# Optimization experiments

Measured on AMD Instinct MI355X. Metric: run time of the kernel, lower is better.

The kernel has to match this reference:

```python
import jax, jax.numpy as jnp
import numpy as np

N = 100000
E = 1600000
IN_DIM = 32
LATENT = 64
K = 3          # num_hops
L = 5          # num_layers


def setup_inputs() -> dict:
    key = jax.random.key(0)
    ks = jax.random.split(key, 8)
    x = jax.random.normal(ks[0], (N, IN_DIM), dtype=jnp.float32)
    edge_index = jax.random.randint(ks[1], (2, E), 0, N, dtype=jnp.int64)
    edge_weight = jax.random.uniform(ks[2], (E,), dtype=jnp.float32)
    # TAGConv params: per layer, (K+1) hop-wise linear weights + one bias
    s0 = 1.0 / np.sqrt(IN_DIM)
    s1 = 1.0 / np.sqrt(LATENT)
    W0 = jax.random.uniform(ks[3], (K + 1, IN_DIM, LATENT), jnp.float32, -s0, s0)
    b0 = jnp.zeros((LATENT,), jnp.float32)
    Ws = jax.random.uniform(ks[4], (L - 1, K + 1, LATENT, LATENT), jnp.float32, -s1, s1)
    bs = jnp.zeros((L - 1, LATENT), jnp.float32)
    return {"x": x, "edge_index": edge_index, "edge_weight": edge_weight,
            "W0": W0, "b0": b0, "Ws": Ws, "bs": bs}


def _gcn_norm(edge_index, edge_weight, num_nodes):
    # TAGConv uses gcn_norm with add_self_loops=False (symmetric normalization)
    row, col = edge_index[0], edge_index[1]
    deg = jax.ops.segment_sum(edge_weight, col, num_segments=num_nodes)
    safe = jnp.where(deg > 0, deg, 1.0)
    dinv = jnp.where(deg > 0, 1.0 / jnp.sqrt(safe), 0.0)
    return dinv[row] * edge_weight * dinv[col]


def _tagconv(x, row, col, norm, W, b, num_nodes):
    # out = sum_{k=0}^{K} (A_hat^k x) @ W[k] + b
    out = x @ W[0]
    h = x
    for k in range(1, W.shape[0]):
        h = jax.ops.segment_sum(norm[:, None] * h[row], col, num_segments=num_nodes)
        out = out + h @ W[k]
    return out + b


def reference(x, edge_index, edge_weight, W0, b0, Ws, bs):
    row, col = edge_index[0], edge_index[1]
    norm = _gcn_norm(edge_index, edge_weight, N)
    h = jax.nn.relu(_tagconv(x, row, col, norm, W0, b0, N))
    for i in range(Ws.shape[0]):
        h = jax.nn.relu(_tagconv(h, row, col, norm, Ws[i], bs[i], N))
    return h
```

## Files before the change

### kernel.cpp

```cpp
#include <hip/hip_runtime.h>
#include <hip/hip_fp16.h>

#define NN 100000
#define NE 1600000
#define NBKT 196
#define BSH 9
#define BCAP 9216
#define NCOL (NBKT * 512)
#define EPB_A 4096

typedef __half half_t;
using f16x8 = __attribute__((ext_vector_type(8))) _Float16;
using f32x4 = __attribute__((ext_vector_type(4))) float;


__device__ inline float4 load4(const float* p) {
    return *reinterpret_cast<const float4*>(p);
}
__device__ inline float4 load4(const half_t* p) {
    uint2 u = *reinterpret_cast<const uint2*>(p);
    __half2 a = *reinterpret_cast<__half2*>(&u.x);
    __half2 b = *reinterpret_cast<__half2*>(&u.y);
    float2 fa = __half22float2(a), fb = __half22float2(b);
    return make_float4(fa.x, fa.y, fb.x, fb.y);
}
__device__ inline void store_half4(half_t* p, float4 v) {
    __half2 a = __floats2half2_rn(v.x, v.y);
    __half2 b = __floats2half2_rn(v.z, v.w);
    uint2 u;
    u.x = *reinterpret_cast<unsigned*>(&a);
    u.y = *reinterpret_cast<unsigned*>(&b);
    *reinterpret_cast<uint2*>(p) = u;
}


__global__ void f32_to_f16(const float* __restrict__ in, half_t* __restrict__ out, int nquad) {
    int i = blockIdx.x * blockDim.x + threadIdx.x;
    if (i < nquad) store_half4(out + i * 4, load4(in + i * 4));
}

__global__ __launch_bounds__(256) void passA_bucket(
    const int* __restrict__ row, const int* __restrict__ col, const float* __restrict__ w,
    unsigned* __restrict__ gcur, int2* __restrict__ gbkt, int E)
{
    __shared__ unsigned cnt[256];
    __shared__ unsigned lofs[256];
    __shared__ unsigned lcur[256];
    __shared__ unsigned gb[256];
    __shared__ int2 arena[EPB_A];
    __shared__ unsigned short abkt[EPB_A];
    int t = threadIdx.x;
    int base = blockIdx.x * EPB_A;
    int nloc = min(EPB_A, E - base);
    cnt[t] = 0; lcur[t] = 0;
    __syncthreads();
    for (int i = t; i < nloc; i += 256)
        atomicAdd(&cnt[col[base + i] >> BSH], 1u);
    __syncthreads();
    unsigned v = cnt[t];
    lofs[t] = v; __syncthreads();
    for (int d = 1; d < 256; d <<= 1) {
        unsigned u = (t >= d) ? lofs[t - d] : 0u;
        __syncthreads();
        lofs[t] += u;
        __syncthreads();
    }
    unsigned excl = lofs[t] - v;
    __syncthreads();
    lofs[t] = excl;
    __syncthreads();
    if (t < NBKT && cnt[t] > 0) gb[t] = atomicAdd(&gcur[t], cnt[t]);
    for (int i = t; i < nloc; i += 256) {
        int e = base + i;
        int c = col[e];
        int b = c >> BSH;
        unsigned p = lofs[b] + atomicAdd(&lcur[b], 1u);
        unsigned packed = ((unsigned)(c & 511) << 17) | (unsigned)row[e];
        arena[p] = make_int2((int)packed, __float_as_int(w[e]));
        abkt[p] = (unsigned short)b;
    }
    __syncthreads();
    for (int i = t; i < nloc; i += 256) {
        int b = abkt[i];
        unsigned j = i - lofs[b];
        gbkt[(size_t)b * BCAP + gb[b] + j] = arena[i];
    }
}

__global__ __launch_bounds__(256) void passB_hist(
    const int2* __restrict__ gbkt, const unsigned* __restrict__ gcur,
    unsigned* __restrict__ cnt, float* __restrict__ deg)
{
    __shared__ unsigned c512[512];
    __shared__ float d512[512];
    int t = threadIdx.x;
    int b = blockIdx.x;
    for (int i = t; i < 512; i += 256) { c512[i] = 0; d512[i] = 0.f; }
    __syncthreads();
    unsigned sz = min(gcur[b], (unsigned)BCAP);
    const int2* src = gbkt + (size_t)b * BCAP;
    for (unsigned i = t; i < sz; i += 256) {
        int2 v = src[i];
        unsigned colw = ((unsigned)v.x) >> 17;
        atomicAdd(&c512[colw], 1u);
        atomicAdd(&d512[colw], __int_as_float(v.y));
    }
    __syncthreads();
    for (int i = t; i < 512; i += 256) {
        cnt[b * 512 + i] = c512[i];
        deg[b * 512 + i] = d512[i];
    }
}

__global__ void dinv_kernel(const float* __restrict__ deg, float* __restrict__ dinv, int n) {
    int i = blockIdx.x * blockDim.x + threadIdx.x;
    if (i < n) {
        float d = deg[i];
        dinv[i] = d > 0.f ? rsqrtf(d) : 0.f;
    }
}

__global__ void scan_phase1(const unsigned* __restrict__ cnt, unsigned* __restrict__ bsum, int n) {
    __shared__ unsigned sh[256];
    int t = threadIdx.x;
    int base = blockIdx.x * 1024 + t * 4;
    unsigned s = 0;
#pragma unroll
    for (int j = 0; j < 4; j++) { int i = base + j; if (i < n) s += cnt[i]; }
    sh[t] = s; __syncthreads();
    for (int d = 128; d > 0; d >>= 1) {
        if (t < d) sh[t] += sh[t + d];
        __syncthreads();
    }
    if (t == 0) bsum[blockIdx.x] = sh[0];
}

__global__ void scan_phase2(const unsigned* __restrict__ bsum, unsigned* __restrict__ bbase, int nb) {
    __shared__ unsigned sh[128];
    int t = threadIdx.x;
    unsigned v = (t < nb) ? bsum[t] : 0u;
    sh[t] = v; __syncthreads();
    for (int d = 1; d < 128; d <<= 1) {
        unsigned u = (t >= d) ? sh[t - d] : 0u;
        __syncthreads();
        sh[t] += u;
        __syncthreads();
    }
    if (t < nb) bbase[t] = sh[t] - v;
}

__global__ void scan_phase3(const unsigned* __restrict__ cnt, const unsigned* __restrict__ bbase,
                            unsigned* __restrict__ offsets, int n) {
    __shared__ unsigned sh[256];
    int t = threadIdx.x;
    int base = blockIdx.x * 1024 + t * 4;
    unsigned c[4]; unsigned s = 0;
#pragma unroll
    for (int j = 0; j < 4; j++) { int i = base + j; c[j] = (i < n) ? cnt[i] : 0u; s += c[j]; }
    sh[t] = s; __syncthreads();
    for (int d = 1; d < 256; d <<= 1) {
        unsigned u = (t >= d) ? sh[t - d] : 0u;
        __syncthreads();
        sh[t] += u;
        __syncthreads();
    }
    unsigned o = bbase[blockIdx.x] + sh[t] - s;
#pragma unroll
    for (int j = 0; j < 4; j++) {
        int i = base + j;
        if (i < n) { offsets[i] = o; o += c[j]; }
    }
}

__global__ __launch_bounds__(256) void passC_place(
    const int2* __restrict__ gbkt, const unsigned* __restrict__ gcur,
    const unsigned* __restrict__ offsets, const float* __restrict__ dinv,
    int2* __restrict__ ent)
{
    __shared__ unsigned lcur[512];
    int t = threadIdx.x;
    int b = blockIdx.x;
    for (int i = t; i < 512; i += 256) lcur[i] = 0;
    __syncthreads();
    unsigned sz = min(gcur[b], (unsigned)BCAP);
    const int2* src = gbkt + (size_t)b * BCAP;
    for (unsigned i = t; i < sz; i += 256) {
        int2 v = src[i];
        unsigned colw = ((unsigned)v.x) >> 17;
        int r = v.x & 0x1FFFF;
        int c = (b << BSH) | (int)colw;
        unsigned pos = offsets[c] + atomicAdd(&lcur[colw], 1u);
        float wv = __int_as_float(v.y) * dinv[r];
        ent[pos] = make_int2(r, __float_as_int(wv));
    }
}


template <int DIM, typename SrcT>
__global__ __launch_bounds__(256) void spmm_kernel(
    const SrcT* __restrict__ src, half_t* __restrict__ pout,
    const int2* __restrict__ ent, const unsigned* __restrict__ offs,
    const unsigned* __restrict__ cnt, const float* __restrict__ dinv, int n)
{
    constexpr int TPN = DIM / 4;
    constexpr int NPB = 256 / TPN;
    int node = blockIdx.x * NPB + threadIdx.x / TPN;
    int f = (threadIdx.x % TPN) * 4;
    if (node >= n) return;
    unsigned off = offs[node];
    unsigned c = cnt[node];
    float dv = dinv[node];
    float4 a = {0.f, 0.f, 0.f, 0.f};
#pragma unroll 2
    for (unsigned e = off; e < off + c; ++e) {
        int2 en = ent[e];
        float w = __int_as_float(en.y);
        float4 v = load4(src + (size_t)en.x * DIM + f);
        a.x += w * v.x; a.y += w * v.y; a.z += w * v.z; a.w += w * v.w;
    }
    a.x *= dv; a.y *= dv; a.z *= dv; a.w *= dv;
    store_half4(pout + (size_t)node * DIM + f, a);
}


__global__ __launch_bounds__(256) void spmm64_kernel(
    const half_t* __restrict__ src, half_t* __restrict__ pout,
    const int2* __restrict__ ent, const unsigned* __restrict__ offs,
    const unsigned* __restrict__ cnt, const float* __restrict__ dinv, int n)
{
    int node = blockIdx.x * 32 + (threadIdx.x >> 3);
    int f = (threadIdx.x & 7) * 8;
    if (node >= n) return;
    unsigned off = offs[node], c = cnt[node];
    float dv = dinv[node];
    float acc[8] = {};
#pragma unroll 2
    for (unsigned e = off; e < off + c; ++e) {
        int2 en = ent[e];
        float w = __int_as_float(en.y);
        uint4 raw = *reinterpret_cast<const uint4*>(src + (size_t)en.x * 64 + f);
        __half2* h2 = reinterpret_cast<__half2*>(&raw);
#pragma unroll
        for (int j = 0; j < 4; ++j) {
            float2 v = __half22float2(h2[j]);
            acc[2 * j]     += w * v.x;
            acc[2 * j + 1] += w * v.y;
        }
    }
    uint4 o;
    __half2 h;
    h = __floats2half2_rn(acc[0] * dv, acc[1] * dv); o.x = *reinterpret_cast<unsigned*>(&h);
    h = __floats2half2_rn(acc[2] * dv, acc[3] * dv); o.y = *reinterpret_cast<unsigned*>(&h);
    h = __floats2half2_rn(acc[4] * dv, acc[5] * dv); o.z = *reinterpret_cast<unsigned*>(&h);
    h = __floats2half2_rn(acc[6] * dv, acc[7] * dv); o.w = *reinterpret_cast<unsigned*>(&h);
    *reinterpret_cast<uint4*>(pout + (size_t)node * 64 + f) = o;
}


template <int IN, int MODE>
__global__ __launch_bounds__(256) void fused4_mfma(
    const half_t* __restrict__ A0, const half_t* __restrict__ P1,
    const half_t* __restrict__ P2, const half_t* __restrict__ P3,
    const float* __restrict__ W, const float* __restrict__ bias,
    half_t* __restrict__ hdst, float* __restrict__ fdst, int n)
{
    constexpr int KK  = IN / 32;
    constexpr int WTS = IN + 8;
    __shared__ _Float16 Wt[64][WTS];
    int t = threadIdx.x;
    int w = t >> 6, l = t & 63;
    int nodeBase = blockIdx.x * 64;
    int rowTop = nodeBase + w * 16;

    f32x4 acc[4];
#pragma unroll
    for (int ct = 0; ct < 4; ++ct) acc[ct] = (f32x4){0.f, 0.f, 0.f, 0.f};

    int row = rowTop + (l & 15);
    if (row >= n) row = n - 1;
    const int khome = (l >> 4) * 8;

#pragma unroll
    for (int s = 0; s < 4; ++s) {
        const half_t* S = (s == 0) ? A0 : (s == 1) ? P1 : (s == 2) ? P2 : P3;
        const float* Wsrc = W + s * IN * 64;
        for (int idx = t; idx < IN * 64; idx += 256) {
            int k = idx >> 6, colj = idx & 63;
            Wt[colj][k] = (_Float16)Wsrc[idx];
        }
        __syncthreads();
#pragma unroll
        for (int kk = 0; kk < KK; ++kk) {
            uint4 araw = *reinterpret_cast<const uint4*>(S + (size_t)row * IN + kk * 32 + khome);
            f16x8 afrag = __builtin_bit_cast(f16x8, araw);
#pragma unroll
            for (int ct = 0; ct < 4; ++ct) {
                f16x8 bfrag = *reinterpret_cast<const f16x8*>(&Wt[ct * 16 + (l & 15)][kk * 32 + khome]);
                acc[ct] = __builtin_amdgcn_mfma_f32_16x16x32_f16(afrag, bfrag, acc[ct], 0, 0, 0);
            }
        }
        __syncthreads();
    }

    int colb = l & 15;
    int rbase = rowTop + (l >> 4) * 4;
#pragma unroll
    for (int ct = 0; ct < 4; ++ct) {
#pragma unroll
        for (int r = 0; r < 4; ++r) {
            int node = rbase + r;
            if (node >= n) continue;
            int colj = ct * 16 + colb;
            float v = fmaxf(acc[ct][r] + bias[colj], 0.f);
            size_t o = (size_t)node * 64 + colj;
            if (MODE == 1) hdst[o] = __float2half_rn(v);
            else           fdst[o] = v;
        }
    }
}


extern "C" void kernel_launch(void* const* d_in, const int* in_sizes, int n_in,
                              void* d_out, int out_size, void* d_ws, size_t ws_size,
                              hipStream_t stream) {
    const float* x  = (const float*)d_in[0];
    const int*   ei = (const int*)d_in[1];
    const float* ew = (const float*)d_in[2];
    const float* W0 = (const float*)d_in[3];
    const float* b0 = (const float*)d_in[4];
    const float* Ws = (const float*)d_in[5];
    const float* bs = (const float*)d_in[6];
    float* out = (float*)d_out;

    const int* row = ei;
    const int* col = ei + NE;

    char* wsp = (char*)d_ws;
    auto alloc = [&](size_t bytes) -> char* {
        char* p = wsp;
        wsp += (bytes + 255) & ~(size_t)255;
        return p;
    };
    float*    dinv    = (float*)alloc((size_t)NCOL * 4);
    float*    deg     = (float*)alloc((size_t)NCOL * 4);
    unsigned* cnt     = (unsigned*)alloc((size_t)NCOL * 4);
    unsigned* offsets = (unsigned*)alloc((size_t)NCOL * 4);
    unsigned* bsum    = (unsigned*)alloc(256 * 4);
    unsigned* bbase   = (unsigned*)alloc(256 * 4);
    unsigned* gcur    = (unsigned*)alloc(NBKT * 4);
    int2*     ent     = (int2*)alloc((size_t)NE * 8);
    half_t*   xh      = (half_t*)alloc((size_t)NN * 32 * 2);
    half_t*   B0      = (half_t*)alloc((size_t)NN * 64 * 2);
    half_t*   P1      = (half_t*)alloc((size_t)NN * 64 * 2);
    half_t*   P2      = (half_t*)alloc((size_t)NN * 64 * 2);
    half_t*   P3      = (half_t*)alloc((size_t)NN * 64 * 2);
    int2*     gbkt    = (int2*)P1;

    hipMemsetAsync(gcur, 0, NBKT * 4, stream);

    f32_to_f16<<<(NN * 32 / 4 + 255) / 256, 256, 0, stream>>>(x, xh, NN * 32 / 4);

    const int AB = (NE + EPB_A - 1) / EPB_A;
    passA_bucket<<<AB, 256, 0, stream>>>(row, col, ew, gcur, gbkt, NE);
    passB_hist<<<NBKT, 256, 0, stream>>>(gbkt, gcur, cnt, deg);
    dinv_kernel<<<(NN + 255) / 256, 256, 0, stream>>>(deg, dinv, NN);
    const int NB = NCOL / 1024;
    scan_phase1<<<NB, 256, 0, stream>>>(cnt, bsum, NCOL);
    scan_phase2<<<1, 128, 0, stream>>>(bsum, bbase, NB);
    scan_phase3<<<NB, 256, 0, stream>>>(cnt, bbase, offsets, NCOL);
    passC_place<<<NBKT, 256, 0, stream>>>(gbkt, gcur, offsets, dinv, ent);

    const int MMB  = (NN + 63) / 64;
    const int SB32 = (NN + 31) / 32;
    const int SB64 = (NN + 31) / 32;

    spmm_kernel<32, float><<<SB32, 256, 0, stream>>>(x, P1, ent, offsets, cnt, dinv, NN);
    spmm_kernel<32, half_t><<<SB32, 256, 0, stream>>>(P1, P2, ent, offsets, cnt, dinv, NN);
    spmm_kernel<32, half_t><<<SB32, 256, 0, stream>>>(P2, P3, ent, offsets, cnt, dinv, NN);
    fused4_mfma<32, 1><<<MMB, 256, 0, stream>>>(xh, P1, P2, P3, W0, b0, B0, nullptr, NN);

    for (int l = 0; l < 4; ++l) {
        const float* Wl = Ws + (size_t)l * 4 * 64 * 64;
        const float* bl = bs + (size_t)l * 64;
        spmm64_kernel<<<SB64, 256, 0, stream>>>(B0, P1, ent, offsets, cnt, dinv, NN);
        spmm64_kernel<<<SB64, 256, 0, stream>>>(P1, P2, ent, offsets, cnt, dinv, NN);
        spmm64_kernel<<<SB64, 256, 0, stream>>>(P2, P3, ent, offsets, cnt, dinv, NN);
        if (l < 3)
            fused4_mfma<64, 1><<<MMB, 256, 0, stream>>>(B0, P1, P2, P3, Wl, bl, B0, nullptr, NN);
        else
            fused4_mfma<64, 2><<<MMB, 256, 0, stream>>>(B0, P1, P2, P3, Wl, bl, nullptr, out, NN);
    }
}
```

Measured before the change: 664.1 us.

## Sort nodes by in-degree to balance SpMM warp workloads

Adds a degree histogram, a scan and a permutation-build pass that order nodes into buckets by in-degree (capped at 63). All SpMM kernels then process nodes through this permutation, so the nodes sharing a wavefront have similar edge counts and less lane divergence in the edge loop. The cost is three extra small kernels, an indirection load per node, and scattered output writes, which lose the locality of nodes being stored in index order.

```diff
diff --git a/kernel.cpp b/kernel.cpp
--- a/kernel.cpp
+++ b/kernel.cpp
@@ -196,17 +196,64 @@
 }
 
 
-template <int DIM, typename SrcT>
-__global__ __launch_bounds__(256) void spmm_kernel(
+__global__ __launch_bounds__(256) void deg_hist(const unsigned* __restrict__ cnt,
+                                                unsigned* __restrict__ dhist, int n) {
+    __shared__ unsigned h[64];
+    int t = threadIdx.x;
+    if (t < 64) h[t] = 0;
+    __syncthreads();
+    int i = blockIdx.x * 256 + t;
+    if (i < n) atomicAdd(&h[min(cnt[i], 63u)], 1u);
+    __syncthreads();
+    if (t < 64 && h[t]) atomicAdd(&dhist[t], h[t]);
+}
+
+__global__ void deg_scan(const unsigned* __restrict__ dhist, unsigned* __restrict__ dcur) {
+    __shared__ unsigned sh[64];
+    int t = threadIdx.x;
+    unsigned v = dhist[t];
+    sh[t] = v; __syncthreads();
+    for (int d = 1; d < 64; d <<= 1) {
+        unsigned u = (t >= d) ? sh[t - d] : 0u;
+        __syncthreads();
+        sh[t] += u;
+        __syncthreads();
+    }
+    dcur[t] = sh[t] - v;
+}
+
+__global__ __launch_bounds__(256) void perm_build(const unsigned* __restrict__ cnt,
+                                                  unsigned* __restrict__ dcur,
+                                                  int* __restrict__ perm, int n) {
+    __shared__ unsigned h[64], gb[64], lc[64];
+    int t = threadIdx.x;
+    if (t < 64) { h[t] = 0; lc[t] = 0; }
+    __syncthreads();
+    int i = blockIdx.x * 256 + t;
+    bool valid = i < n;
+    unsigned b = 0;
+    if (valid) { b = min(cnt[i], 63u); atomicAdd(&h[b], 1u); }
+    __syncthreads();
+    if (t < 64 && h[t]) gb[t] = atomicAdd(&dcur[t], h[t]);
+    __syncthreads();
+    if (valid) {
+        unsigned r = atomicAdd(&lc[b], 1u);
+        perm[gb[b] + r] = i;
+    }
+}
+
+
+template <typename SrcT>
+__global__ __launch_bounds__(256) void spmm32_kernel(
     const SrcT* __restrict__ src, half_t* __restrict__ pout,
     const int2* __restrict__ ent, const unsigned* __restrict__ offs,
-    const unsigned* __restrict__ cnt, const float* __restrict__ dinv, int n)
-{
-    constexpr int TPN = DIM / 4;
-    constexpr int NPB = 256 / TPN;
-    int node = blockIdx.x * NPB + threadIdx.x / TPN;
-    int f = (threadIdx.x % TPN) * 4;
-    if (node >= n) return;
+    const unsigned* __restrict__ cnt, const float* __restrict__ dinv,
+    const int* __restrict__ perm, int n)
+{
+    int s = blockIdx.x * 32 + (threadIdx.x >> 3);
+    int f = (threadIdx.x & 7) * 4;
+    if (s >= n) return;
+    int node = perm[s];
     unsigned off = offs[node];
     unsigned c = cnt[node];
     float dv = dinv[node];
@@ -215,22 +262,24 @@
     for (unsigned e = off; e < off + c; ++e) {
         int2 en = ent[e];
         float w = __int_as_float(en.y);
-        float4 v = load4(src + (size_t)en.x * DIM + f);
+        float4 v = load4(src + (size_t)en.x * 32 + f);
         a.x += w * v.x; a.y += w * v.y; a.z += w * v.z; a.w += w * v.w;
     }
     a.x *= dv; a.y *= dv; a.z *= dv; a.w *= dv;
-    store_half4(pout + (size_t)node * DIM + f, a);
+    store_half4(pout + (size_t)node * 32 + f, a);
 }
 
 
 __global__ __launch_bounds__(256) void spmm64_kernel(
     const half_t* __restrict__ src, half_t* __restrict__ pout,
     const int2* __restrict__ ent, const unsigned* __restrict__ offs,
-    const unsigned* __restrict__ cnt, const float* __restrict__ dinv, int n)
-{
-    int node = blockIdx.x * 32 + (threadIdx.x >> 3);
+    const unsigned* __restrict__ cnt, const float* __restrict__ dinv,
+    const int* __restrict__ perm, int n)
+{
+    int s = blockIdx.x * 32 + (threadIdx.x >> 3);
     int f = (threadIdx.x & 7) * 8;
-    if (node >= n) return;
+    if (s >= n) return;
+    int node = perm[s];
     unsigned off = offs[node], c = cnt[node];
     float dv = dinv[node];
     float acc[8] = {};
@@ -345,9 +394,12 @@
     float*    deg     = (float*)alloc((size_t)NCOL * 4);
     unsigned* cnt     = (unsigned*)alloc((size_t)NCOL * 4);
     unsigned* offsets = (unsigned*)alloc((size_t)NCOL * 4);
+    int*      perm    = (int*)alloc((size_t)NN * 4);
     unsigned* bsum    = (unsigned*)alloc(256 * 4);
     unsigned* bbase   = (unsigned*)alloc(256 * 4);
     unsigned* gcur    = (unsigned*)alloc(NBKT * 4);
+    unsigned* dhist   = (unsigned*)alloc(64 * 4);
+    unsigned* dcur    = (unsigned*)alloc(64 * 4);
     int2*     ent     = (int2*)alloc((size_t)NE * 8);
     half_t*   xh      = (half_t*)alloc((size_t)NN * 32 * 2);
     half_t*   B0      = (half_t*)alloc((size_t)NN * 64 * 2);
@@ -357,6 +409,7 @@
     int2*     gbkt    = (int2*)P1;
 
     hipMemsetAsync(gcur, 0, NBKT * 4, stream);
+    hipMemsetAsync(dhist, 0, 64 * 4, stream);
 
     f32_to_f16<<<(NN * 32 / 4 + 255) / 256, 256, 0, stream>>>(x, xh, NN * 32 / 4);
 
@@ -364,27 +417,30 @@
     passA_bucket<<<AB, 256, 0, stream>>>(row, col, ew, gcur, gbkt, NE);
     passB_hist<<<NBKT, 256, 0, stream>>>(gbkt, gcur, cnt, deg);
     dinv_kernel<<<(NN + 255) / 256, 256, 0, stream>>>(deg, dinv, NN);
+    const int PB = (NN + 255) / 256;
+    deg_hist<<<PB, 256, 0, stream>>>(cnt, dhist, NN);
+    deg_scan<<<1, 64, 0, stream>>>(dhist, dcur);
+    perm_build<<<PB, 256, 0, stream>>>(cnt, dcur, perm, NN);
     const int NB = NCOL / 1024;
     scan_phase1<<<NB, 256, 0, stream>>>(cnt, bsum, NCOL);
     scan_phase2<<<1, 128, 0, stream>>>(bsum, bbase, NB);
     scan_phase3<<<NB, 256, 0, stream>>>(cnt, bbase, offsets, NCOL);
     passC_place<<<NBKT, 256, 0, stream>>>(gbkt, gcur, offsets, dinv, ent);
 
-    const int MMB  = (NN + 63) / 64;
-    const int SB32 = (NN + 31) / 32;
-    const int SB64 = (NN + 31) / 32;
-
-    spmm_kernel<32, float><<<SB32, 256, 0, stream>>>(x, P1, ent, offsets, cnt, dinv, NN);
-    spmm_kernel<32, half_t><<<SB32, 256, 0, stream>>>(P1, P2, ent, offsets, cnt, dinv, NN);
-    spmm_kernel<32, half_t><<<SB32, 256, 0, stream>>>(P2, P3, ent, offsets, cnt, dinv, NN);
+    const int MMB = (NN + 63) / 64;
+    const int SB  = (NN + 31) / 32;
+
+    spmm32_kernel<float><<<SB, 256, 0, stream>>>(x, P1, ent, offsets, cnt, dinv, perm, NN);
+    spmm32_kernel<half_t><<<SB, 256, 0, stream>>>(P1, P2, ent, offsets, cnt, dinv, perm, NN);
+    spmm32_kernel<half_t><<<SB, 256, 0, stream>>>(P2, P3, ent, offsets, cnt, dinv, perm, NN);
     fused4_mfma<32, 1><<<MMB, 256, 0, stream>>>(xh, P1, P2, P3, W0, b0, B0, nullptr, NN);
 
     for (int l = 0; l < 4; ++l) {
         const float* Wl = Ws + (size_t)l * 4 * 64 * 64;
         const float* bl = bs + (size_t)l * 64;
-        spmm64_kernel<<<SB64, 256, 0, stream>>>(B0, P1, ent, offsets, cnt, dinv, NN);
-        spmm64_kernel<<<SB64, 256, 0, stream>>>(P1, P2, ent, offsets, cnt, dinv, NN);
-        spmm64_kernel<<<SB64, 256, 0, stream>>>(P2, P3, ent, offsets, cnt, dinv, NN);
+        spmm64_kernel<<<SB, 256, 0, stream>>>(B0, P1, ent, offsets, cnt, dinv, perm, NN);
+        spmm64_kernel<<<SB, 256, 0, stream>>>(P1, P2, ent, offsets, cnt, dinv, perm, NN);
+        spmm64_kernel<<<SB, 256, 0, stream>>>(P2, P3, ent, offsets, cnt, dinv, perm, NN);
         if (l < 3)
             fused4_mfma<64, 1><<<MMB, 256, 0, stream>>>(B0, P1, P2, P3, Wl, bl, B0, nullptr, NN);
         else
```

After: 711.1 us. 7.1% more time.
